# Kernel tuning notes

Hardware: AMD Instinct MI355X
Metric: run time of the kernel (lower is better)

## Reference

```python
import jax, jax.numpy as jnp
import numpy as np

N = 50000
E = 800000
IN_DIM = 256
HID = 256
LAT = 64
H1 = 4
H2 = 4
O1 = HID // H1  # 64 per-head out of conv1
NEG_SLOPE = 0.2


def setup_inputs() -> dict:
    key = jax.random.key(0)
    ks = jax.random.split(key, 12)
    x = jax.random.normal(ks[0], (N, IN_DIM), dtype=jnp.float32)
    edge_index = jax.random.randint(ks[1], (2, E), 0, N, dtype=jnp.int64)
    g = lambda k, shape: jax.random.normal(k, shape, dtype=jnp.float32) * (1.0 / np.sqrt(shape[-1]))
    W1 = g(ks[2], (IN_DIM, H1 * O1))
    a_src1 = g(ks[3], (H1, O1))
    a_dst1 = g(ks[4], (H1, O1))
    b1 = jnp.zeros((H1 * O1,), dtype=jnp.float32)
    W2 = g(ks[5], (HID, H2 * LAT))
    a_src2 = g(ks[6], (H2, LAT))
    a_dst2 = g(ks[7], (H2, LAT))
    b2 = jnp.zeros((LAT,), dtype=jnp.float32)
    return {"x": x, "edge_index": edge_index, "W1": W1, "a_src1": a_src1,
            "a_dst1": a_dst1, "b1": b1, "W2": W2, "a_src2": a_src2,
            "a_dst2": a_dst2, "b2": b2}


def _gat_conv(x, src, dst, W, a_src, a_dst, bias, concat):
    # src/dst already include self-loops. x: (N, F_in)
    n, heads, out = x.shape[0], a_src.shape[0], a_src.shape[1]
    h = (x @ W).reshape(n, heads, out)                      # (N,H,O)
    al_src = jnp.einsum('nho,ho->nh', h, a_src)             # (N,H)
    al_dst = jnp.einsum('nho,ho->nh', h, a_dst)
    e = al_src[src] + al_dst[dst]                           # (Et,H)
    e = jnp.where(e > 0, e, NEG_SLOPE * e)                  # LeakyReLU(0.2)
    # softmax over incoming edges of each dst node
    m = jax.ops.segment_max(e, dst, num_segments=n)         # (N,H)
    p = jnp.exp(e - m[dst])
    denom = jax.ops.segment_sum(p, dst, num_segments=n)     # (N,H)
    alpha = p / denom[dst]                                  # (Et,H)
    msg = h[src] * alpha[:, :, None]                        # (Et,H,O)
    out_n = jax.ops.segment_sum(msg, dst, num_segments=n)   # (N,H,O)
    if concat:
        out_n = out_n.reshape(n, heads * out)
    else:
        out_n = out_n.mean(axis=1)
    return out_n + bias


def reference(x, edge_index, W1, a_src1, a_dst1, b1, W2, a_src2, a_dst2, b2):
    src, dst = edge_index[0], edge_index[1]
    # add self-loops (PyG GATConv default)
    loops = jnp.arange(N, dtype=edge_index.dtype)
    src_sl = jnp.concatenate([src, loops])
    dst_sl = jnp.concatenate([dst, loops])
    h = _gat_conv(x, src_sl, dst_sl, W1, a_src1, a_dst1, b1, concat=True)
    h = jax.nn.elu(h)
    z = _gat_conv(h, src_sl, dst_sl, W2, a_src2, a_dst2, b2, concat=False)
    # DotDecoder on original edge_index
    logits = jnp.einsum('ed,ed->e', z[src], z[dst])
    return logits
```

## Files before the change

### kernel.cpp

```cpp
#include <hip/hip_runtime.h>
#include <math.h>

#define N_NODES 50000
#define E_EDGES 800000
#define DIM 256
#define HEADS 4
#define HO 64
#define NEG_SLOPE 0.2f
#define SCAN_NBLK ((N_NODES + 255) / 256)

typedef __attribute__((ext_vector_type(8))) short bf16x8;
typedef __attribute__((ext_vector_type(4))) float f32x4;

static __device__ inline ushort f2bf(float f) {
  union { float f; unsigned u; } v; v.f = f;
  unsigned r = (v.u + 0x7fff + ((v.u >> 16) & 1)) >> 16;
  return (ushort)r;
}
static __device__ inline float bf2f(ushort h) {
  union { unsigned u; float f; } v; v.u = ((unsigned)h) << 16;
  return v.f;
}

__global__ __launch_bounds__(256) void cvt_split_T(const float* __restrict__ W,
                                                   ushort* __restrict__ bthi,
                                                   ushort* __restrict__ btlo) {
  int idx = blockIdx.x * 256 + threadIdx.x;
  int k = idx >> 8, n = idx & 255;
  float v = W[idx];
  ushort h = f2bf(v);
  ushort l = f2bf(v - bf2f(h));
  bthi[n * 256 + k] = h;
  btlo[n * 256 + k] = l;
}

#define GBM 128
#define GBK 32
#define LDK 40

__global__ __launch_bounds__(256) void gemm_mfma(const float* __restrict__ A,
                                                 const ushort* __restrict__ Bhi,
                                                 const ushort* __restrict__ Blo,
                                                 ushort* __restrict__ Cbf, int M) {
  __shared__ __align__(16) ushort As[2][GBM][LDK];
  __shared__ __align__(16) ushort Bs[2][GBM][LDK];
  const int tid = threadIdx.x;
  const int lane = tid & 63;
  const int wave = tid >> 6;
  const int row0 = blockIdx.x * GBM;
  const int col0 = blockIdx.y * GBM;
  const int wm = (wave & 1) * 64;
  const int wn = (wave >> 1) * 64;
  const int rA = lane & 15;
  const int kb = (lane >> 4) * 8;

  f32x4 acc[4][4] = {};

  for (int k0 = 0; k0 < DIM; k0 += GBK) {
#pragma unroll
    for (int qq = 0; qq < 4; ++qq) {
      int q = tid + qq * 256;
      int r = q >> 3, c = q & 7;
      int grow = row0 + r;
      float4 v = make_float4(0.f, 0.f, 0.f, 0.f);
      if (grow < M) v = *(const float4*)&A[(size_t)grow * DIM + k0 + c * 4];
      ushort4 h, l;
      h.x = f2bf(v.x); l.x = f2bf(v.x - bf2f(h.x));
      h.y = f2bf(v.y); l.y = f2bf(v.y - bf2f(h.y));
      h.z = f2bf(v.z); l.z = f2bf(v.z - bf2f(h.z));
      h.w = f2bf(v.w); l.w = f2bf(v.w - bf2f(h.w));
      *(ushort4*)&As[0][r][c * 4] = h;
      *(ushort4*)&As[1][r][c * 4] = l;
    }
#pragma unroll
    for (int qq = 0; qq < 2; ++qq) {
      int q = tid + qq * 256;
      int r = q >> 2, c = q & 3;
      bf16x8 wh = *(const bf16x8*)&Bhi[(size_t)(col0 + r) * DIM + k0 + c * 8];
      bf16x8 wl = *(const bf16x8*)&Blo[(size_t)(col0 + r) * DIM + k0 + c * 8];
      *(bf16x8*)&Bs[0][r][c * 8] = wh;
      *(bf16x8*)&Bs[1][r][c * 8] = wl;
    }
    __syncthreads();

    bf16x8 af[2][4], bfr[2][4];
#pragma unroll
    for (int mi = 0; mi < 4; ++mi) {
      af[0][mi] = *(const bf16x8*)&As[0][wm + mi * 16 + rA][kb];
      af[1][mi] = *(const bf16x8*)&As[1][wm + mi * 16 + rA][kb];
    }
#pragma unroll
    for (int ni = 0; ni < 4; ++ni) {
      bfr[0][ni] = *(const bf16x8*)&Bs[0][wn + ni * 16 + rA][kb];
      bfr[1][ni] = *(const bf16x8*)&Bs[1][wn + ni * 16 + rA][kb];
    }
#pragma unroll
    for (int mi = 0; mi < 4; ++mi)
#pragma unroll
      for (int ni = 0; ni < 4; ++ni) {
        acc[mi][ni] = __builtin_amdgcn_mfma_f32_16x16x32_bf16(af[0][mi], bfr[0][ni], acc[mi][ni], 0, 0, 0);
        acc[mi][ni] = __builtin_amdgcn_mfma_f32_16x16x32_bf16(af[0][mi], bfr[1][ni], acc[mi][ni], 0, 0, 0);
        acc[mi][ni] = __builtin_amdgcn_mfma_f32_16x16x32_bf16(af[1][mi], bfr[0][ni], acc[mi][ni], 0, 0, 0);
      }
    __syncthreads();
  }

#pragma unroll
  for (int mi = 0; mi < 4; ++mi) {
    int rbase = row0 + wm + mi * 16 + (lane >> 4) * 4;
#pragma unroll
    for (int ni = 0; ni < 4; ++ni) {
      int col = col0 + wn + ni * 16 + (lane & 15);
#pragma unroll
      for (int r = 0; r < 4; ++r) {
        int row = rbase + r;
        if (row < M) Cbf[(size_t)row * DIM + col] = f2bf(acc[mi][ni][r]);
      }
    }
  }
}

__global__ __launch_bounds__(256) void attn_logits(const ushort* __restrict__ h,
                                                   const float* __restrict__ a_src,
                                                   const float* __restrict__ a_dst,
                                                   float* __restrict__ al_s,
                                                   float* __restrict__ al_d) {
  int gid = blockIdx.x * blockDim.x + threadIdx.x;
  int node = gid >> 6;
  int lane = threadIdx.x & 63;
  if (node >= N_NODES) return;
  ushort4 hv = *(const ushort4*)&h[(size_t)node * DIM + lane * 4];
  float4 as = *(const float4*)&a_src[lane * 4];
  float4 ad = *(const float4*)&a_dst[lane * 4];
  float h0 = bf2f(hv.x), h1 = bf2f(hv.y), h2 = bf2f(hv.z), h3 = bf2f(hv.w);
  float s = h0 * as.x + h1 * as.y + h2 * as.z + h3 * as.w;
  float d = h0 * ad.x + h1 * ad.y + h2 * ad.z + h3 * ad.w;
#pragma unroll
  for (int off = 8; off >= 1; off >>= 1) {
    s += __shfl_xor(s, off, 64);
    d += __shfl_xor(d, off, 64);
  }
  if ((lane & 15) == 0) {
    int head = lane >> 4;
    al_s[node * HEADS + head] = s;
    al_d[node * HEADS + head] = d;
  }
}

__global__ __launch_bounds__(256) void histo(const int* __restrict__ dst, int* __restrict__ deg) {
  int e = blockIdx.x * blockDim.x + threadIdx.x;
  if (e < E_EDGES) atomicAdd(&deg[dst[e]], 1);
}

__global__ __launch_bounds__(256) void scan1(const int* __restrict__ deg,
                                             int* __restrict__ excl,
                                             int* __restrict__ blockSums) {
  __shared__ int tmp[256];
  int i = blockIdx.x * 256 + threadIdx.x;
  int v = (i < N_NODES) ? deg[i] : 0;
  tmp[threadIdx.x] = v;
  __syncthreads();
  for (int off = 1; off < 256; off <<= 1) {
    int t = (threadIdx.x >= off) ? tmp[threadIdx.x - off] : 0;
    __syncthreads();
    tmp[threadIdx.x] += t;
    __syncthreads();
  }
  int incl = tmp[threadIdx.x];
  if (i < N_NODES) excl[i] = incl - v;
  if (threadIdx.x == 255) blockSums[blockIdx.x] = incl;
}

__global__ __launch_bounds__(256) void scan2(int* __restrict__ blockSums) {
  __shared__ int tmp[256];
  int i = threadIdx.x;
  int v = (i < SCAN_NBLK) ? blockSums[i] : 0;
  tmp[i] = v;
  __syncthreads();
  for (int off = 1; off < 256; off <<= 1) {
    int t = (i >= off) ? tmp[i - off] : 0;
    __syncthreads();
    tmp[i] += t;
    __syncthreads();
  }
  if (i < SCAN_NBLK) blockSums[i] = tmp[i] - v;
}

__global__ __launch_bounds__(256) void scan3(int* __restrict__ excl,
                                             const int* __restrict__ blockSums,
                                             int* __restrict__ cursor) {
  int i = blockIdx.x * 256 + threadIdx.x;
  if (i < N_NODES) {
    int r = excl[i] + blockSums[blockIdx.x];
    excl[i] = r;
    cursor[i] = r;
  }
}

__global__ __launch_bounds__(256) void scatter(const int* __restrict__ src,
                                               const int* __restrict__ dst,
                                               int* __restrict__ cursor,
                                               int* __restrict__ csr_src) {
  int e = blockIdx.x * blockDim.x + threadIdx.x;
  if (e >= E_EDGES) return;
  int pos = atomicAdd(&cursor[dst[e]], 1);
  csr_src[pos] = src[e];
}

#define AGG_BODY(S)                                                         \
  {                                                                         \
    float e0 = als[(S) * HEADS + head] + aldv;                              \
    e0 = e0 > 0.f ? e0 : NEG_SLOPE * e0;                                    \
    float p = __expf(e0);                                                   \
    bf16x8 hv = *(const bf16x8*)&hbf[(size_t)(S) * DIM + c0];               \
    den += p;                                                               \
    acc[0] += p * bf2f((ushort)hv[0]);                                      \
    acc[1] += p * bf2f((ushort)hv[1]);                                      \
    acc[2] += p * bf2f((ushort)hv[2]);                                      \
    acc[3] += p * bf2f((ushort)hv[3]);                                      \
    acc[4] += p * bf2f((ushort)hv[4]);                                      \
    acc[5] += p * bf2f((ushort)hv[5]);                                      \
    acc[6] += p * bf2f((ushort)hv[6]);                                      \
    acc[7] += p * bf2f((ushort)hv[7]);                                      \
  }

__global__ __launch_bounds__(256) void agg1(const int* __restrict__ rowptr,
                                            const int* __restrict__ csr_src,
                                            const ushort* __restrict__ hbf,
                                            const float* __restrict__ als,
                                            const float* __restrict__ ald,
                                            const float* __restrict__ bias,
                                            float* __restrict__ x2) {
  int gid = blockIdx.x * blockDim.x + threadIdx.x;
  int node = gid >> 6;
  if (node >= N_NODES) return;
  int lane = threadIdx.x & 63;
  int li = lane & 31, half = lane >> 5;
  int head = li >> 3;
  int c0 = li * 8;
  int rs = rowptr[node];
  int deg = ((node < N_NODES - 1) ? rowptr[node + 1] : E_EDGES) - rs;
  float aldv = ald[node * HEADS + head];
  float den = 0.f;
  float acc[8] = {};
  int total = deg + 1;
  int it = half;
  for (; it + 2 < total; it += 4) {
    int s0 = csr_src[rs + it];
    int s1 = (it + 2 < deg) ? csr_src[rs + it + 2] : node;
    AGG_BODY(s0)
    AGG_BODY(s1)
  }
  for (; it < total; it += 2) {
    int s0 = (it < deg) ? csr_src[rs + it] : node;
    AGG_BODY(s0)
  }
  den += __shfl_xor(den, 32, 64);
#pragma unroll
  for (int j = 0; j < 8; ++j) acc[j] += __shfl_xor(acc[j], 32, 64);
  if (half == 0) {
    float inv = 1.f / den;
    float r[8];
#pragma unroll
    for (int j = 0; j < 8; ++j) {
      r[j] = acc[j] * inv + bias[c0 + j];
      r[j] = r[j] > 0.f ? r[j] : expm1f(r[j]);
    }
    *(float4*)&x2[(size_t)node * DIM + c0] = make_float4(r[0], r[1], r[2], r[3]);
    *(float4*)&x2[(size_t)node * DIM + c0 + 4] = make_float4(r[4], r[5], r[6], r[7]);
  }
}

__global__ __launch_bounds__(256) void agg2(const int* __restrict__ rowptr,
                                            const int* __restrict__ csr_src,
                                            const ushort* __restrict__ hbf,
                                            const float* __restrict__ als,
                                            const float* __restrict__ ald,
                                            const float* __restrict__ b2,
                                            float* __restrict__ z) {
  int gid = blockIdx.x * blockDim.x + threadIdx.x;
  int node = gid >> 6;
  if (node >= N_NODES) return;
  int lane = threadIdx.x & 63;
  int li = lane & 31, half = lane >> 5;
  int head = li >> 3;
  int c0 = li * 8;
  int rs = rowptr[node];
  int deg = ((node < N_NODES - 1) ? rowptr[node + 1] : E_EDGES) - rs;
  float aldv = ald[node * HEADS + head];
  float den = 0.f;
  float acc[8] = {};
  int total = deg + 1;
  int it = half;
  for (; it + 2 < total; it += 4) {
    int s0 = csr_src[rs + it];
    int s1 = (it + 2 < deg) ? csr_src[rs + it + 2] : node;
    AGG_BODY(s0)
    AGG_BODY(s1)
  }
  for (; it < total; it += 2) {
    int s0 = (it < deg) ? csr_src[rs + it] : node;
    AGG_BODY(s0)
  }
  den += __shfl_xor(den, 32, 64);
#pragma unroll
  for (int j = 0; j < 8; ++j) acc[j] += __shfl_xor(acc[j], 32, 64);
  float inv = 1.f / den;
  float r[8];
#pragma unroll
  for (int j = 0; j < 8; ++j) {
    r[j] = acc[j] * inv;
    r[j] += __shfl_xor(r[j], 8, 64);
    r[j] += __shfl_xor(r[j], 16, 64);
  }
  if (lane < 8) {
    int zc = li * 8;
    float4 v0 = make_float4(r[0] * 0.25f + b2[zc + 0], r[1] * 0.25f + b2[zc + 1],
                            r[2] * 0.25f + b2[zc + 2], r[3] * 0.25f + b2[zc + 3]);
    float4 v1 = make_float4(r[4] * 0.25f + b2[zc + 4], r[5] * 0.25f + b2[zc + 5],
                            r[6] * 0.25f + b2[zc + 6], r[7] * 0.25f + b2[zc + 7]);
    *(float4*)&z[(size_t)node * HO + zc] = v0;
    *(float4*)&z[(size_t)node * HO + zc + 4] = v1;
  }
}

__global__ __launch_bounds__(256) void decoder(const int* __restrict__ src,
                                               const int* __restrict__ dst,
                                               const float* __restrict__ z,
                                               float* __restrict__ out) {
  long long gid = (long long)blockIdx.x * blockDim.x + threadIdx.x;
  int e = (int)(gid >> 4);
  if (e >= E_EDGES) return;
  int l = threadIdx.x & 15;
  int s = src[e];
  int d = dst[e];
  float4 a = *(const float4*)&z[(size_t)s * HO + l * 4];
  float4 b = *(const float4*)&z[(size_t)d * HO + l * 4];
  float v = a.x * b.x + a.y * b.y + a.z * b.z + a.w * b.w;
#pragma unroll
  for (int off = 8; off >= 1; off >>= 1) v += __shfl_xor(v, off, 64);
  if (l == 0) out[e] = v;
}

extern "C" void kernel_launch(void* const* d_in, const int* in_sizes, int n_in,
                              void* d_out, int out_size, void* d_ws, size_t ws_size,
                              hipStream_t stream) {
  const float* x      = (const float*)d_in[0];
  const int*   ei     = (const int*)d_in[1];
  const float* W1     = (const float*)d_in[2];
  const float* a_src1 = (const float*)d_in[3];
  const float* a_dst1 = (const float*)d_in[4];
  const float* b1     = (const float*)d_in[5];
  const float* W2     = (const float*)d_in[6];
  const float* a_src2 = (const float*)d_in[7];
  const float* a_dst2 = (const float*)d_in[8];
  const float* b2     = (const float*)d_in[9];
  const int* src = ei;
  const int* dst = ei + E_EDGES;
  float* logits = (float*)d_out;

  float* x2fp = (float*)d_ws;
  float* zlat = x2fp + (size_t)N_NODES * DIM;
  float* als1 = zlat + (size_t)N_NODES * HO;
  float* ald1 = als1 + N_NODES * HEADS;
  float* als2 = ald1 + N_NODES * HEADS;
  float* ald2 = als2 + N_NODES * HEADS;
  int* deg      = (int*)(ald2 + N_NODES * HEADS);
  int* rowptr   = deg + N_NODES;
  int* cursor   = rowptr + N_NODES;
  int* blockSums= cursor + N_NODES;
  int* csr_src  = blockSums + 256;
  ushort* hbf   = (ushort*)(csr_src + E_EDGES);
  ushort* bthi  = hbf + (size_t)N_NODES * DIM;
  ushort* btlo  = bthi + DIM * DIM;

  dim3 blk(256);
  dim3 gemmGrid((N_NODES + GBM - 1) / GBM, DIM / GBM);
  int nodeBlocks = (N_NODES * 64 + 255) / 256;
  int edgeThreadBlocks = (E_EDGES + 255) / 256;
  int decBlocks  = (int)(((long long)E_EDGES * 16 + 255) / 256);

  hipMemsetAsync(deg, 0, N_NODES * sizeof(int), stream);
  hipLaunchKernelGGL(histo, dim3(edgeThreadBlocks), blk, 0, stream, dst, deg);
  hipLaunchKernelGGL(scan1, dim3(SCAN_NBLK), blk, 0, stream, deg, rowptr, blockSums);
  hipLaunchKernelGGL(scan2, dim3(1), blk, 0, stream, blockSums);
  hipLaunchKernelGGL(scan3, dim3(SCAN_NBLK), blk, 0, stream, rowptr, blockSums, cursor);
  hipLaunchKernelGGL(scatter, dim3(edgeThreadBlocks), blk, 0, stream, src, dst, cursor, csr_src);

  hipLaunchKernelGGL(cvt_split_T, dim3(DIM * DIM / 256), blk, 0, stream, W1, bthi, btlo);
  hipLaunchKernelGGL(gemm_mfma, gemmGrid, blk, 0, stream, x, bthi, btlo, hbf, N_NODES);
  hipLaunchKernelGGL(attn_logits, dim3(nodeBlocks), blk, 0, stream, hbf, a_src1, a_dst1, als1, ald1);
  hipLaunchKernelGGL(agg1, dim3(nodeBlocks), blk, 0, stream, rowptr, csr_src, hbf, als1, ald1, b1, x2fp);

  hipLaunchKernelGGL(cvt_split_T, dim3(DIM * DIM / 256), blk, 0, stream, W2, bthi, btlo);
  hipLaunchKernelGGL(gemm_mfma, gemmGrid, blk, 0, stream, x2fp, bthi, btlo, hbf, N_NODES);
  hipLaunchKernelGGL(attn_logits, dim3(nodeBlocks), blk, 0, stream, hbf, a_src2, a_dst2, als2, ald2);
  hipLaunchKernelGGL(agg2, dim3(nodeBlocks), blk, 0, stream, rowptr, csr_src, hbf, als2, ald2, b2, zlat);

  hipLaunchKernelGGL(decoder, dim3(decBlocks), blk, 0, stream, src, dst, zlat, logits);
}
```

Baseline: 417.3 us.

## Split aggregation wave into four edge groups with software-prefetched gathers

The aggregation kernels now split each 64-lane wave into four 16-lane groups. Each group handles every fourth incoming edge and each lane covers 16 bf16 features instead of 8. The gather loop is software-pipelined: the next edge's index, attention logit and feature row load are issued before the current edge is accumulated, to hide gather latency. The bf16 unpack is done with shifts and masks. In exchange, register use and cross-lane shuffle reductions roughly double.

```diff
diff --git a/kernel.cpp b/kernel.cpp
--- a/kernel.cpp
+++ b/kernel.cpp
@@ -207,22 +207,59 @@
   csr_src[pos] = src[e];
 }
 
-#define AGG_BODY(S)                                                         \
-  {                                                                         \
-    float e0 = als[(S) * HEADS + head] + aldv;                              \
-    e0 = e0 > 0.f ? e0 : NEG_SLOPE * e0;                                    \
-    float p = __expf(e0);                                                   \
-    bf16x8 hv = *(const bf16x8*)&hbf[(size_t)(S) * DIM + c0];               \
-    den += p;                                                               \
-    acc[0] += p * bf2f((ushort)hv[0]);                                      \
-    acc[1] += p * bf2f((ushort)hv[1]);                                      \
-    acc[2] += p * bf2f((ushort)hv[2]);                                      \
-    acc[3] += p * bf2f((ushort)hv[3]);                                      \
-    acc[4] += p * bf2f((ushort)hv[4]);                                      \
-    acc[5] += p * bf2f((ushort)hv[5]);                                      \
-    acc[6] += p * bf2f((ushort)hv[6]);                                      \
-    acc[7] += p * bf2f((ushort)hv[7]);                                      \
-  }
+__device__ __forceinline__ void agg_gather(int node, int g, int pos, int head,
+                                           const int* __restrict__ rowptr,
+                                           const int* __restrict__ csr_src,
+                                           const ushort* __restrict__ hbf,
+                                           const float* __restrict__ als,
+                                           float aldv,
+                                           float& den, float (&acc)[16]) {
+  int rs = rowptr[node];
+  int deg = ((node < N_NODES - 1) ? rowptr[node + 1] : E_EDGES) - rs;
+  int total = deg + 1;
+  int c0 = pos * 16;
+
+  bool v0 = g < total;
+  int s0 = node;
+  if (v0 && g < deg) s0 = csr_src[rs + g];
+  float al0 = als[s0 * HEADS + head];
+  const ushort* hp0 = &hbf[(size_t)s0 * DIM + c0];
+  bf16x8 ha0 = *(const bf16x8*)hp0;
+  bf16x8 hb0 = *(const bf16x8*)(hp0 + 8);
+
+  for (int it = g; it < total; it += 4) {
+    int nit = it + 4;
+    bool v1 = nit < total;
+    int s1 = node;
+    if (v1 && nit < deg) s1 = csr_src[rs + nit];
+    float al1 = als[s1 * HEADS + head];
+    const ushort* hp1 = &hbf[(size_t)s1 * DIM + c0];
+    bf16x8 ha1 = *(const bf16x8*)hp1;
+    bf16x8 hb1 = *(const bf16x8*)(hp1 + 8);
+
+    float e0 = al0 + aldv;
+    e0 = e0 > 0.f ? e0 : NEG_SLOPE * e0;
+    float p = v0 ? __expf(e0) : 0.f;
+    den += p;
+    const uint* ua = (const uint*)&ha0;
+    const uint* ub = (const uint*)&hb0;
+#pragma unroll
+    for (int q = 0; q < 4; ++q) {
+      float flo = __uint_as_float(ua[q] << 16);
+      float fhi = __uint_as_float(ua[q] & 0xffff0000u);
+      acc[2 * q]     += p * flo;
+      acc[2 * q + 1] += p * fhi;
+    }
+#pragma unroll
+    for (int q = 0; q < 4; ++q) {
+      float flo = __uint_as_float(ub[q] << 16);
+      float fhi = __uint_as_float(ub[q] & 0xffff0000u);
+      acc[8 + 2 * q]     += p * flo;
+      acc[8 + 2 * q + 1] += p * fhi;
+    }
+    v0 = v1; al0 = al1; ha0 = ha1; hb0 = hb1;
+  }
+}
 
 __global__ __launch_bounds__(256) void agg1(const int* __restrict__ rowptr,
                                             const int* __restrict__ csr_src,
@@ -235,39 +272,34 @@
   int node = gid >> 6;
   if (node >= N_NODES) return;
   int lane = threadIdx.x & 63;
-  int li = lane & 31, half = lane >> 5;
-  int head = li >> 3;
-  int c0 = li * 8;
-  int rs = rowptr[node];
-  int deg = ((node < N_NODES - 1) ? rowptr[node + 1] : E_EDGES) - rs;
+  int g = lane >> 4, pos = lane & 15;
+  int head = pos >> 2;
   float aldv = ald[node * HEADS + head];
   float den = 0.f;
-  float acc[8] = {};
-  int total = deg + 1;
-  int it = half;
-  for (; it + 2 < total; it += 4) {
-    int s0 = csr_src[rs + it];
-    int s1 = (it + 2 < deg) ? csr_src[rs + it + 2] : node;
-    AGG_BODY(s0)
-    AGG_BODY(s1)
-  }
-  for (; it < total; it += 2) {
-    int s0 = (it < deg) ? csr_src[rs + it] : node;
-    AGG_BODY(s0)
-  }
+  float acc[16] = {};
+  agg_gather(node, g, pos, head, rowptr, csr_src, hbf, als, aldv, den, acc);
+
+  den += __shfl_xor(den, 16, 64);
   den += __shfl_xor(den, 32, 64);
 #pragma unroll
-  for (int j = 0; j < 8; ++j) acc[j] += __shfl_xor(acc[j], 32, 64);
-  if (half == 0) {
+  for (int j = 0; j < 16; ++j) {
+    acc[j] += __shfl_xor(acc[j], 16, 64);
+    acc[j] += __shfl_xor(acc[j], 32, 64);
+  }
+  if (g == 0) {
+    int c0 = pos * 16;
     float inv = 1.f / den;
-    float r[8];
-#pragma unroll
-    for (int j = 0; j < 8; ++j) {
+    float r[16];
+#pragma unroll
+    for (int j = 0; j < 16; ++j) {
       r[j] = acc[j] * inv + bias[c0 + j];
       r[j] = r[j] > 0.f ? r[j] : expm1f(r[j]);
     }
-    *(float4*)&x2[(size_t)node * DIM + c0] = make_float4(r[0], r[1], r[2], r[3]);
-    *(float4*)&x2[(size_t)node * DIM + c0 + 4] = make_float4(r[4], r[5], r[6], r[7]);
+#pragma unroll
+    for (int q = 0; q < 4; ++q) {
+      *(float4*)&x2[(size_t)node * DIM + c0 + q * 4] =
+          make_float4(r[4 * q], r[4 * q + 1], r[4 * q + 2], r[4 * q + 3]);
+    }
   }
 }
 
@@ -282,45 +314,38 @@
   int node = gid >> 6;
   if (node >= N_NODES) return;
   int lane = threadIdx.x & 63;
-  int li = lane & 31, half = lane >> 5;
-  int head = li >> 3;
-  int c0 = li * 8;
-  int rs = rowptr[node];
-  int deg = ((node < N_NODES - 1) ? rowptr[node + 1] : E_EDGES) - rs;
+  int g = lane >> 4, pos = lane & 15;
+  int head = pos >> 2;
   float aldv = ald[node * HEADS + head];
   float den = 0.f;
-  float acc[8] = {};
-  int total = deg + 1;
-  int it = half;
-  for (; it + 2 < total; it += 4) {
-    int s0 = csr_src[rs + it];
-    int s1 = (it + 2 < deg) ? csr_src[rs + it + 2] : node;
-    AGG_BODY(s0)
-    AGG_BODY(s1)
-  }
-  for (; it < total; it += 2) {
-    int s0 = (it < deg) ? csr_src[rs + it] : node;
-    AGG_BODY(s0)
-  }
+  float acc[16] = {};
+  agg_gather(node, g, pos, head, rowptr, csr_src, hbf, als, aldv, den, acc);
+
+  den += __shfl_xor(den, 16, 64);
   den += __shfl_xor(den, 32, 64);
 #pragma unroll
-  for (int j = 0; j < 8; ++j) acc[j] += __shfl_xor(acc[j], 32, 64);
+  for (int j = 0; j < 16; ++j) {
+    acc[j] += __shfl_xor(acc[j], 16, 64);
+    acc[j] += __shfl_xor(acc[j], 32, 64);
+  }
   float inv = 1.f / den;
-  float r[8];
-#pragma unroll
-  for (int j = 0; j < 8; ++j) {
+  float r[16];
+#pragma unroll
+  for (int j = 0; j < 16; ++j) {
     r[j] = acc[j] * inv;
+    r[j] += __shfl_xor(r[j], 4, 64);
     r[j] += __shfl_xor(r[j], 8, 64);
-    r[j] += __shfl_xor(r[j], 16, 64);
-  }
-  if (lane < 8) {
-    int zc = li * 8;
-    float4 v0 = make_float4(r[0] * 0.25f + b2[zc + 0], r[1] * 0.25f + b2[zc + 1],
-                            r[2] * 0.25f + b2[zc + 2], r[3] * 0.25f + b2[zc + 3]);
-    float4 v1 = make_float4(r[4] * 0.25f + b2[zc + 4], r[5] * 0.25f + b2[zc + 5],
-                            r[6] * 0.25f + b2[zc + 6], r[7] * 0.25f + b2[zc + 7]);
-    *(float4*)&z[(size_t)node * HO + zc] = v0;
-    *(float4*)&z[(size_t)node * HO + zc + 4] = v1;
+  }
+  if (lane < 4) {
+    int zc = pos * 16;
+#pragma unroll
+    for (int q = 0; q < 4; ++q) {
+      float4 v = make_float4(r[4 * q] * 0.25f + b2[zc + 4 * q],
+                             r[4 * q + 1] * 0.25f + b2[zc + 4 * q + 1],
+                             r[4 * q + 2] * 0.25f + b2[zc + 4 * q + 2],
+                             r[4 * q + 3] * 0.25f + b2[zc + 4 * q + 3]);
+      *(float4*)&z[(size_t)node * HO + zc + q * 4] = v;
+    }
   }
 }
 
```

Result: no change. 420.7 us (+0.8%).

## Fuse attention-logit dot products into GEMM epilogue and merge weight conversions

Applied to the files above, without the earlier changes.

Computes the per-head source and destination attention logits inside the MFMA GEMM epilogue from the fp32 accumulators. It uses lane shuffles plus atomicAdd into zeroed buffers, which removes the separate attn_logits kernel that re-read the bf16 h matrix. The two weight split/transpose conversions are merged into one launch writing separate buffers. In exchange it adds a memset, atomics and extra epilogue work. Logits now come from unrounded accumulators, so they differ slightly from before.

```diff
diff --git a/kernel.cpp b/kernel.cpp
--- a/kernel.cpp
+++ b/kernel.cpp
@@ -22,16 +22,23 @@
   return v.f;
 }
 
-__global__ __launch_bounds__(256) void cvt_split_T(const float* __restrict__ W,
-                                                   ushort* __restrict__ bthi,
-                                                   ushort* __restrict__ btlo) {
-  int idx = blockIdx.x * 256 + threadIdx.x;
+__global__ __launch_bounds__(256) void cvt_split_T2(const float* __restrict__ W1,
+                                                    const float* __restrict__ W2,
+                                                    ushort* __restrict__ bt1hi,
+                                                    ushort* __restrict__ bt1lo,
+                                                    ushort* __restrict__ bt2hi,
+                                                    ushort* __restrict__ bt2lo) {
+  int gidx = blockIdx.x * 256 + threadIdx.x;
+  const float* W = (gidx < DIM * DIM) ? W1 : W2;
+  ushort* bhi = (gidx < DIM * DIM) ? bt1hi : bt2hi;
+  ushort* blo = (gidx < DIM * DIM) ? bt1lo : bt2lo;
+  int idx = gidx & (DIM * DIM - 1);
   int k = idx >> 8, n = idx & 255;
   float v = W[idx];
   ushort h = f2bf(v);
   ushort l = f2bf(v - bf2f(h));
-  bthi[n * 256 + k] = h;
-  btlo[n * 256 + k] = l;
+  bhi[n * 256 + k] = h;
+  blo[n * 256 + k] = l;
 }
 
 #define GBM 128
@@ -41,7 +48,12 @@
 __global__ __launch_bounds__(256) void gemm_mfma(const float* __restrict__ A,
                                                  const ushort* __restrict__ Bhi,
                                                  const ushort* __restrict__ Blo,
-                                                 ushort* __restrict__ Cbf, int M) {
+                                                 ushort* __restrict__ Cbf,
+                                                 const float* __restrict__ a_src,
+                                                 const float* __restrict__ a_dst,
+                                                 float* __restrict__ als,
+                                                 float* __restrict__ ald,
+                                                 int M) {
   __shared__ __align__(16) ushort As[2][GBM][LDK];
   __shared__ __align__(16) ushort Bs[2][GBM][LDK];
   const int tid = threadIdx.x;
@@ -118,32 +130,37 @@
       }
     }
   }
-}
-
-__global__ __launch_bounds__(256) void attn_logits(const ushort* __restrict__ h,
-                                                   const float* __restrict__ a_src,
-                                                   const float* __restrict__ a_dst,
-                                                   float* __restrict__ al_s,
-                                                   float* __restrict__ al_d) {
-  int gid = blockIdx.x * blockDim.x + threadIdx.x;
-  int node = gid >> 6;
-  int lane = threadIdx.x & 63;
-  if (node >= N_NODES) return;
-  ushort4 hv = *(const ushort4*)&h[(size_t)node * DIM + lane * 4];
-  float4 as = *(const float4*)&a_src[lane * 4];
-  float4 ad = *(const float4*)&a_dst[lane * 4];
-  float h0 = bf2f(hv.x), h1 = bf2f(hv.y), h2 = bf2f(hv.z), h3 = bf2f(hv.w);
-  float s = h0 * as.x + h1 * as.y + h2 * as.z + h3 * as.w;
-  float d = h0 * ad.x + h1 * ad.y + h2 * ad.z + h3 * ad.w;
-#pragma unroll
-  for (int off = 8; off >= 1; off >>= 1) {
-    s += __shfl_xor(s, off, 64);
-    d += __shfl_xor(d, off, 64);
-  }
-  if ((lane & 15) == 0) {
-    int head = lane >> 4;
-    al_s[node * HEADS + head] = s;
-    al_d[node * HEADS + head] = d;
+
+  const int head = (col0 + wn) >> 6;
+  float coefS[4], coefD[4];
+#pragma unroll
+  for (int ni = 0; ni < 4; ++ni) {
+    int o = ni * 16 + (lane & 15);
+    coefS[ni] = a_src[head * HO + o];
+    coefD[ni] = a_dst[head * HO + o];
+  }
+#pragma unroll
+  for (int mi = 0; mi < 4; ++mi) {
+    int rbase = row0 + wm + mi * 16 + (lane >> 4) * 4;
+#pragma unroll
+    for (int r = 0; r < 4; ++r) {
+      float s = 0.f, d = 0.f;
+#pragma unroll
+      for (int ni = 0; ni < 4; ++ni) {
+        s += acc[mi][ni][r] * coefS[ni];
+        d += acc[mi][ni][r] * coefD[ni];
+      }
+#pragma unroll
+      for (int off = 1; off <= 8; off <<= 1) {
+        s += __shfl_xor(s, off, 64);
+        d += __shfl_xor(d, off, 64);
+      }
+      int row = rbase + r;
+      if ((lane & 15) == 0 && row < M) {
+        atomicAdd(&als[row * HEADS + head], s);
+        atomicAdd(&ald[row * HEADS + head], d);
+      }
+    }
   }
 }
 
@@ -371,8 +388,10 @@
   int* blockSums= cursor + N_NODES;
   int* csr_src  = blockSums + 256;
   ushort* hbf   = (ushort*)(csr_src + E_EDGES);
-  ushort* bthi  = hbf + (size_t)N_NODES * DIM;
-  ushort* btlo  = bthi + DIM * DIM;
+  ushort* bt1hi = hbf + (size_t)N_NODES * DIM;
+  ushort* bt1lo = bt1hi + DIM * DIM;
+  ushort* bt2hi = bt1lo + DIM * DIM;
+  ushort* bt2lo = bt2hi + DIM * DIM;
 
   dim3 blk(256);
   dim3 gemmGrid((N_NODES + GBM - 1) / GBM, DIM / GBM);
@@ -380,21 +399,24 @@
   int edgeThreadBlocks = (E_EDGES + 255) / 256;
   int decBlocks  = (int)(((long long)E_EDGES * 16 + 255) / 256);
 
+  hipMemsetAsync(als1, 0, (size_t)4 * N_NODES * HEADS * sizeof(float), stream);
   hipMemsetAsync(deg, 0, N_NODES * sizeof(int), stream);
+
   hipLaunchKernelGGL(histo, dim3(edgeThreadBlocks), blk, 0, stream, dst, deg);
   hipLaunchKernelGGL(scan1, dim3(SCAN_NBLK), blk, 0, stream, deg, rowptr, blockSums);
   hipLaunchKernelGGL(scan2, dim3(1), blk, 0, stream, blockSums);
   hipLaunchKernelGGL(scan3, dim3(SCAN_NBLK), blk, 0, stream, rowptr, blockSums, cursor);
   hipLaunchKernelGGL(scatter, dim3(edgeThreadBlocks), blk, 0, stream, src, dst, cursor, csr_src);
 
-  hipLaunchKernelGGL(cvt_split_T, dim3(DIM * DIM / 256), blk, 0, stream, W1, bthi, btlo);
-  hipLaunchKernelGGL(gemm_mfma, gemmGrid, blk, 0, stream, x, bthi, btlo, hbf, N_NODES);
-  hipLaunchKernelGGL(attn_logits, dim3(nodeBlocks), blk, 0, stream, hbf, a_src1, a_dst1, als1, ald1);
+  hipLaunchKernelGGL(cvt_split_T2, dim3(2 * DIM * DIM / 256), blk, 0, stream,
+                     W1, W2, bt1hi, bt1lo, bt2hi, bt2lo);
+
+  hipLaunchKernelGGL(gemm_mfma, gemmGrid, blk, 0, stream, x, bt1hi, bt1lo, hbf,
+                     a_src1, a_dst1, als1, ald1, N_NODES);
   hipLaunchKernelGGL(agg1, dim3(nodeBlocks), blk, 0, stream, rowptr, csr_src, hbf, als1, ald1, b1, x2fp);
 
-  hipLaunchKernelGGL(cvt_split_T, dim3(DIM * DIM / 256), blk, 0, stream, W2, bthi, btlo);
-  hipLaunchKernelGGL(gemm_mfma, gemmGrid, blk, 0, stream, x2fp, bthi, btlo, hbf, N_NODES);
-  hipLaunchKernelGGL(attn_logits, dim3(nodeBlocks), blk, 0, stream, hbf, a_src2, a_dst2, als2, ald2);
+  hipLaunchKernelGGL(gemm_mfma, gemmGrid, blk, 0, stream, x2fp, bt2hi, bt2lo, hbf,
+                     a_src2, a_dst2, als2, ald2, N_NODES);
   hipLaunchKernelGGL(agg2, dim3(nodeBlocks), blk, 0, stream, rowptr, csr_src, hbf, als2, ald2, b2, zlat);
 
   hipLaunchKernelGGL(decoder, dim3(decBlocks), blk, 0, stream, src, dst, zlat, logits);
```

Result: slower. 442.8 us (+6.1%).
